# Kernel optimization log

Measured on AMD Instinct MI355X. Metric: run time of the kernel, lower is better.

Reference implementation:

```python
import jax, jax.numpy as jnp
import numpy as np

N, NFEAT, NHID, NCLASS = 10000, 512, 256, 16
CRF_ITERS = 3


def setup_inputs() -> dict:
    key = jax.random.key(0)
    ks = jax.random.split(key, 10)
    x = jax.random.normal(ks[0], (N, NFEAT), dtype=jnp.float32)
    # sparse-ish adjacency: ~50 neighbors/node, self-loops, row-normalized (GCN style)
    mask = (jax.random.uniform(ks[1], (N, N)) < 0.005).astype(jnp.float32)
    adj = mask + jnp.eye(N, dtype=jnp.float32)
    adj = adj / jnp.sum(adj, axis=1, keepdims=True)
    s1 = 1.0 / np.sqrt(NFEAT)
    s2 = 1.0 / np.sqrt(NHID)
    W1 = jax.random.normal(ks[2], (NFEAT, NHID), dtype=jnp.float32) * s1
    b1 = jnp.zeros((NHID,), dtype=jnp.float32)
    Wq = jax.random.normal(ks[3], (NHID, NHID), dtype=jnp.float32) * s2
    Wk = jax.random.normal(ks[4], (NHID, NHID), dtype=jnp.float32) * s2
    alpha = jnp.float32(1.0)
    beta = jnp.float32(1.0)
    ln_w = jnp.ones((NHID,), dtype=jnp.float32)
    ln_b = jnp.zeros((NHID,), dtype=jnp.float32)
    W2 = jax.random.normal(ks[5], (NHID, NCLASS), dtype=jnp.float32) * s2
    b2 = jnp.zeros((NCLASS,), dtype=jnp.float32)
    return {"x": x, "adj": adj, "W1": W1, "b1": b1, "Wq": Wq, "Wk": Wk,
            "alpha": alpha, "beta": beta, "ln_w": ln_w, "ln_b": ln_b,
            "W2": W2, "b2": b2}


def reference(x, adj, W1, b1, Wq, Wk, alpha, beta, ln_w, ln_b, W2, b2):
    # gc1: adj @ (x W1) + b1, then relu
    h = jax.nn.relu(adj @ (x @ W1) + b1)          # [N, NHID]
    # CRF_Node: adjacency-masked similarity attention, 3 mean-field iterations
    q = h @ Wq
    k = h @ Wk
    scores = (q @ k.T) / jnp.sqrt(jnp.float32(NHID))  # [N, N]
    logits = jnp.where(adj > 0, scores, jnp.float32(-1e9))
    attn = jax.nn.softmax(logits, axis=-1)
    out = h
    for _ in range(CRF_ITERS):
        out = (alpha * h + beta * (attn @ out)) / (alpha + beta)
    # LayerNorm over feature dim
    mu = jnp.mean(out, axis=-1, keepdims=True)
    var = jnp.var(out, axis=-1, keepdims=True)
    out = (out - mu) * jax.lax.rsqrt(var + 1e-5) * ln_w + ln_b
    # dropout: eval mode (identity)
    # gc2 + log_softmax
    y = adj @ (out @ W2) + b2                     # [N, NCLASS]
    return jax.nn.log_softmax(y, axis=-1)
```

## Files before the change

kernel.cpp:

```cpp
#include <hip/hip_runtime.h>
#include <math.h>
#include <float.h>

#define N_NODES 10000
#define NFEAT   512
#define NHID    256
#define NCLASS  16
#define CAP     128

typedef float nfloat4 __attribute__((ext_vector_type(4)));

__global__ __launch_bounds__(256) void gemm64(const float* __restrict__ A,
                                              const float* __restrict__ B,
                                              float* __restrict__ C,
                                              int M, int K, int N) {
  __shared__ float As[16][68];
  __shared__ float Bs[16][68];
  const int tid  = threadIdx.x;
  const int row0 = blockIdx.x * 64;
  const int col0 = blockIdx.y * 64;
  const int ty = tid >> 4, tx = tid & 15;
  const int arow = tid >> 2;
  const int akq  = (tid & 3) << 2;
  const int brow = tid >> 4;
  const int bcol = (tid & 15) << 2;

  float acc[4][4] = {};
  for (int k0 = 0; k0 < K; k0 += 16) {
    float4 av = make_float4(0.f, 0.f, 0.f, 0.f);
    const int gr = row0 + arow;
    if (gr < M) av = *(const float4*)&A[(size_t)gr * K + k0 + akq];
    As[akq + 0][arow] = av.x;
    As[akq + 1][arow] = av.y;
    As[akq + 2][arow] = av.z;
    As[akq + 3][arow] = av.w;
    const float4 bv = *(const float4*)&B[(size_t)(k0 + brow) * N + col0 + bcol];
    *(float4*)&Bs[brow][bcol] = bv;
    __syncthreads();
#pragma unroll
    for (int k = 0; k < 16; ++k) {
      const float4 a = *(const float4*)&As[k][ty << 2];
      const float4 b = *(const float4*)&Bs[k][tx << 2];
      acc[0][0] += a.x * b.x; acc[0][1] += a.x * b.y; acc[0][2] += a.x * b.z; acc[0][3] += a.x * b.w;
      acc[1][0] += a.y * b.x; acc[1][1] += a.y * b.y; acc[1][2] += a.y * b.z; acc[1][3] += a.y * b.w;
      acc[2][0] += a.z * b.x; acc[2][1] += a.z * b.y; acc[2][2] += a.z * b.z; acc[2][3] += a.z * b.w;
      acc[3][0] += a.w * b.x; acc[3][1] += a.w * b.y; acc[3][2] += a.w * b.z; acc[3][3] += a.w * b.w;
    }
    __syncthreads();
  }
#pragma unroll
  for (int j = 0; j < 4; ++j) {
    const int gr = row0 + (ty << 2) + j;
    if (gr < M) {
      const float4 o = make_float4(acc[j][0], acc[j][1], acc[j][2], acc[j][3]);
      *(float4*)&C[(size_t)gr * N + col0 + (tx << 2)] = o;
    }
  }
}

__global__ __launch_bounds__(256) void wqwkT(const float* __restrict__ Wq,
                                             const float* __restrict__ Wk,
                                             float* __restrict__ Mm) {
  __shared__ float4 qr4[NHID / 4];
  const int a = blockIdx.x, tid = threadIdx.x;
  if (tid < NHID / 4) qr4[tid] = ((const float4*)&Wq[(size_t)a * NHID])[tid];
  __syncthreads();
  const float4* kb = (const float4*)&Wk[(size_t)tid * NHID];
  float acc = 0.f;
#pragma unroll 8
  for (int c4 = 0; c4 < NHID / 4; ++c4) {
    const float4 k4 = kb[c4];
    const float4 q4 = qr4[c4];
    acc += q4.x * k4.x + q4.y * k4.y + q4.z * k4.z + q4.w * k4.w;
  }
  Mm[(size_t)a * NHID + tid] = acc;
}

__global__ __launch_bounds__(256) void scan_build(const float* __restrict__ adj,
                                                  const float* __restrict__ xW1,
                                                  const float* __restrict__ b1,
                                                  int* __restrict__ cols,
                                                  float* __restrict__ vals,
                                                  int* __restrict__ nnz,
                                                  float* __restrict__ h) {
  __shared__ int    lcols[CAP];
  __shared__ float  lvals[CAP];
  __shared__ int    scols[CAP];
  __shared__ float  svals[CAP];
  __shared__ float4 pacc[4][64];
  __shared__ int    cnt;
  const int row = blockIdx.x, tid = threadIdx.x;
  if (tid == 0) cnt = 0;
  __syncthreads();
  const nfloat4* arow = (const nfloat4*)&adj[(size_t)row * N_NODES];
  for (int v = tid; v < N_NODES / 4; v += 256) {
    const nfloat4 f = __builtin_nontemporal_load(&arow[v]);
    if (f.x != 0.f) { int p = atomicAdd(&cnt, 1); if (p < CAP) { lcols[p] = 4 * v + 0; lvals[p] = f.x; } }
    if (f.y != 0.f) { int p = atomicAdd(&cnt, 1); if (p < CAP) { lcols[p] = 4 * v + 1; lvals[p] = f.y; } }
    if (f.z != 0.f) { int p = atomicAdd(&cnt, 1); if (p < CAP) { lcols[p] = 4 * v + 2; lvals[p] = f.z; } }
    if (f.w != 0.f) { int p = atomicAdd(&cnt, 1); if (p < CAP) { lcols[p] = 4 * v + 3; lvals[p] = f.w; } }
  }
  __syncthreads();
  const int c = min(cnt, CAP);
  int myc = 0; float myv = 0.f; int rank = 0;
  if (tid < c) {
    myc = lcols[tid]; myv = lvals[tid];
    for (int e = 0; e < c; ++e) rank += (lcols[e] < myc);
  }
  __syncthreads();
  if (tid < c) { scols[rank] = myc; svals[rank] = myv; }
  __syncthreads();
  if (tid == 0) nnz[row] = c;
  if (tid < c) {
    cols[(size_t)row * CAP + tid] = scols[tid];
    vals[(size_t)row * CAP + tid] = svals[tid];
  }
  const int lane = tid & 63, wv = tid >> 6;
  float4 acc = make_float4(0.f, 0.f, 0.f, 0.f);
  for (int e = wv; e < c; e += 4) {
    const float vv = svals[e];
    const float4 xv = *(const float4*)&xW1[(size_t)scols[e] * NHID + (lane << 2)];
    acc.x += vv * xv.x; acc.y += vv * xv.y; acc.z += vv * xv.z; acc.w += vv * xv.w;
  }
  pacc[wv][lane] = acc;
  __syncthreads();
  if (wv == 0) {
    const float4 p0 = pacc[0][lane], p1 = pacc[1][lane];
    const float4 p2 = pacc[2][lane], p3 = pacc[3][lane];
    const float4 bb = *(const float4*)&b1[lane << 2];
    float4 r;
    r.x = fmaxf(bb.x + ((p0.x + p1.x) + (p2.x + p3.x)), 0.f);
    r.y = fmaxf(bb.y + ((p0.y + p1.y) + (p2.y + p3.y)), 0.f);
    r.z = fmaxf(bb.z + ((p0.z + p1.z) + (p2.z + p3.z)), 0.f);
    r.w = fmaxf(bb.w + ((p0.w + p1.w) + (p2.w + p3.w)), 0.f);
    *(float4*)&h[(size_t)row * NHID + (lane << 2)] = r;
  }
}

__global__ __launch_bounds__(256) void attn_crf1(const float* __restrict__ t,
                                                 const float* __restrict__ h,
                                                 const int* __restrict__ cols,
                                                 const int* __restrict__ nnz,
                                                 float* __restrict__ attn,
                                                 float* __restrict__ outn,
                                                 const float* __restrict__ alpha_p,
                                                 const float* __restrict__ beta_p) {
  __shared__ int   lcols[4][CAP];
  __shared__ float sv[4][CAP];
  const int tid = threadIdx.x, lane = tid & 63, wv = tid >> 6;
  const int row = (blockIdx.x << 2) + wv;
  const int c = nnz[row];
  for (int e = lane; e < c; e += 64) lcols[wv][e] = cols[(size_t)row * CAP + e];
  const int gq = lane >> 4, gl = lane & 15;
  const float* tp = &t[(size_t)row * NHID + (gl << 2)];
  const float4 t0 = *(const float4*)&tp[0];
  const float4 t1 = *(const float4*)&tp[64];
  const float4 t2 = *(const float4*)&tp[128];
  const float4 t3 = *(const float4*)&tp[192];
  for (int e = gq; e < c; e += 4) {
    const float* hp = &h[(size_t)lcols[wv][e] * NHID + (gl << 2)];
    const float4 h0 = *(const float4*)&hp[0];
    const float4 h1 = *(const float4*)&hp[64];
    const float4 h2 = *(const float4*)&hp[128];
    const float4 h3 = *(const float4*)&hp[192];
    float p = t0.x * h0.x + t0.y * h0.y + t0.z * h0.z + t0.w * h0.w
            + t1.x * h1.x + t1.y * h1.y + t1.z * h1.z + t1.w * h1.w
            + t2.x * h2.x + t2.y * h2.y + t2.z * h2.z + t2.w * h2.w
            + t3.x * h3.x + t3.y * h3.y + t3.z * h3.z + t3.w * h3.w;
    p += __shfl_xor(p, 1, 64);
    p += __shfl_xor(p, 2, 64);
    p += __shfl_xor(p, 4, 64);
    p += __shfl_xor(p, 8, 64);
    if (gl == 0) sv[wv][e] = p * 0.0625f;
  }
  const float s1 = (lane      < c) ? sv[wv][lane]      : -FLT_MAX;
  const float s2 = (lane + 64 < c) ? sv[wv][lane + 64] : -FLT_MAX;
  float m = fmaxf(s1, s2);
#pragma unroll
  for (int o = 32; o > 0; o >>= 1) m = fmaxf(m, __shfl_xor(m, o, 64));
  const float e1 = (lane      < c) ? __expf(s1 - m) : 0.f;
  const float e2 = (lane + 64 < c) ? __expf(s2 - m) : 0.f;
  float sum = e1 + e2;
#pragma unroll
  for (int o = 32; o > 0; o >>= 1) sum += __shfl_xor(sum, o, 64);
  const float inv = 1.f / sum;
  if (lane < c) {
    const float aw = e1 * inv;
    sv[wv][lane] = aw;
    attn[(size_t)row * CAP + lane] = aw;
  }
  if (lane + 64 < c) {
    const float aw = e2 * inv;
    sv[wv][lane + 64] = aw;
    attn[(size_t)row * CAP + lane + 64] = aw;
  }
  float4 acc = make_float4(0.f, 0.f, 0.f, 0.f);
  for (int e = 0; e < c; ++e) {
    const float ve = sv[wv][e];
    const float4 xv = *(const float4*)&h[(size_t)lcols[wv][e] * NHID + (lane << 2)];
    acc.x += ve * xv.x; acc.y += ve * xv.y; acc.z += ve * xv.z; acc.w += ve * xv.w;
  }
  const float a = alpha_p[0], b = beta_p[0];
  const float i2 = 1.f / (a + b);
  const float4 hq = *(const float4*)&h[(size_t)row * NHID + (lane << 2)];
  float4 o4;
  o4.x = (a * hq.x + b * acc.x) * i2;
  o4.y = (a * hq.y + b * acc.y) * i2;
  o4.z = (a * hq.z + b * acc.z) * i2;
  o4.w = (a * hq.w + b * acc.w) * i2;
  *(float4*)&outn[(size_t)row * NHID + (lane << 2)] = o4;
}

__global__ __launch_bounds__(256) void crf_iter(const float* __restrict__ h,
                                                const float* __restrict__ attn,
                                                const int* __restrict__ cols,
                                                const int* __restrict__ nnz,
                                                const float* __restrict__ outp,
                                                float* __restrict__ outn,
                                                const float* __restrict__ alpha_p,
                                                const float* __restrict__ beta_p) {
  __shared__ int   lcols[4][CAP];
  __shared__ float lv[4][CAP];
  const int tid = threadIdx.x, lane = tid & 63, wv = tid >> 6;
  const int row = (blockIdx.x << 2) + wv;
  const int c = nnz[row];
  for (int e = lane; e < c; e += 64) {
    lcols[wv][e] = cols[(size_t)row * CAP + e];
    lv[wv][e]   = attn[(size_t)row * CAP + e];
  }
  float4 acc = make_float4(0.f, 0.f, 0.f, 0.f);
  int e = 0;
  for (; e + 1 < c; e += 2) {
    const int   c0 = lcols[wv][e],   c1 = lcols[wv][e + 1];
    const float v0 = lv[wv][e],      v1 = lv[wv][e + 1];
    const float4 x0 = *(const float4*)&outp[(size_t)c0 * NHID + (lane << 2)];
    const float4 x1 = *(const float4*)&outp[(size_t)c1 * NHID + (lane << 2)];
    acc.x += v0 * x0.x; acc.y += v0 * x0.y; acc.z += v0 * x0.z; acc.w += v0 * x0.w;
    acc.x += v1 * x1.x; acc.y += v1 * x1.y; acc.z += v1 * x1.z; acc.w += v1 * x1.w;
  }
  if (e < c) {
    const float ve = lv[wv][e];
    const float4 xv = *(const float4*)&outp[(size_t)lcols[wv][e] * NHID + (lane << 2)];
    acc.x += ve * xv.x; acc.y += ve * xv.y; acc.z += ve * xv.z; acc.w += ve * xv.w;
  }
  const float a = alpha_p[0], b = beta_p[0];
  const float i2 = 1.f / (a + b);
  const float4 hq = *(const float4*)&h[(size_t)row * NHID + (lane << 2)];
  float4 o4;
  o4.x = (a * hq.x + b * acc.x) * i2;
  o4.y = (a * hq.y + b * acc.y) * i2;
  o4.z = (a * hq.z + b * acc.z) * i2;
  o4.w = (a * hq.w + b * acc.w) * i2;
  *(float4*)&outn[(size_t)row * NHID + (lane << 2)] = o4;
}

__global__ __launch_bounds__(256) void crf_ln_w2(const float* __restrict__ h,
                                                 const float* __restrict__ attn,
                                                 const int* __restrict__ cols,
                                                 const int* __restrict__ nnz,
                                                 const float* __restrict__ outp,
                                                 const float* __restrict__ alpha_p,
                                                 const float* __restrict__ beta_p,
                                                 const float* __restrict__ lnw,
                                                 const float* __restrict__ lnb,
                                                 const float* __restrict__ W2,
                                                 float* __restrict__ z) {
  __shared__ int   lcols[4][CAP];
  __shared__ float lv[4][CAP];
  __shared__ float vs[4][NHID];
  __shared__ float part[16][17];
  const int tid = threadIdx.x, lane = tid & 63, wv = tid >> 6;
  const int row = (blockIdx.x << 2) + wv;
  const int c = nnz[row];
  for (int e = lane; e < c; e += 64) {
    lcols[wv][e] = cols[(size_t)row * CAP + e];
    lv[wv][e]   = attn[(size_t)row * CAP + e];
  }
  float4 acc = make_float4(0.f, 0.f, 0.f, 0.f);
  for (int e = 0; e < c; ++e) {
    const float ve = lv[wv][e];
    const float4 xv = *(const float4*)&outp[(size_t)lcols[wv][e] * NHID + (lane << 2)];
    acc.x += ve * xv.x; acc.y += ve * xv.y; acc.z += ve * xv.z; acc.w += ve * xv.w;
  }
  const float a = alpha_p[0], b = beta_p[0];
  const float i2 = 1.f / (a + b);
  const float4 hq = *(const float4*)&h[(size_t)row * NHID + (lane << 2)];
  float4 x4;
  x4.x = (a * hq.x + b * acc.x) * i2;
  x4.y = (a * hq.y + b * acc.y) * i2;
  x4.z = (a * hq.z + b * acc.z) * i2;
  x4.w = (a * hq.w + b * acc.w) * i2;
  float s = x4.x + x4.y + x4.z + x4.w;
#pragma unroll
  for (int o = 32; o > 0; o >>= 1) s += __shfl_xor(s, o, 64);
  const float mu = s * (1.f / NHID);
  float4 d4;
  d4.x = x4.x - mu; d4.y = x4.y - mu; d4.z = x4.z - mu; d4.w = x4.w - mu;
  float v = d4.x * d4.x + d4.y * d4.y + d4.z * d4.z + d4.w * d4.w;
#pragma unroll
  for (int o = 32; o > 0; o >>= 1) v += __shfl_xor(v, o, 64);
  const float rstd = rsqrtf(v * (1.f / NHID) + 1e-5f);
  const float4 lw = *(const float4*)&lnw[lane << 2];
  const float4 lb = *(const float4*)&lnb[lane << 2];
  float4 v4;
  v4.x = d4.x * rstd * lw.x + lb.x;
  v4.y = d4.y * rstd * lw.y + lb.y;
  v4.z = d4.z * rstd * lw.z + lb.z;
  v4.w = d4.w * rstd * lw.w + lb.w;
  *(float4*)&vs[wv][lane << 2] = v4;
  __syncthreads();
  const int g = tid >> 4, cc = tid & 15;
  float w2f[16];
#pragma unroll
  for (int u = 0; u < 16; ++u) w2f[u] = W2[(size_t)((g << 4) + u) * NCLASS + cc];
  for (int rr = 0; rr < 4; ++rr) {
    float p = 0.f;
#pragma unroll
    for (int u = 0; u < 16; ++u) p += vs[rr][(g << 4) + u] * w2f[u];
    part[g][cc] = p;
    __syncthreads();
    if (tid < NCLASS) {
      float q = 0.f;
#pragma unroll
      for (int g2 = 0; g2 < 16; ++g2) q += part[g2][tid];
      z[(size_t)((blockIdx.x << 2) + rr) * NCLASS + tid] = q;
    }
    __syncthreads();
  }
}

__global__ __launch_bounds__(256) void final_k(const float* __restrict__ z,
                                               const float* __restrict__ vals,
                                               const int* __restrict__ cols,
                                               const int* __restrict__ nnz,
                                               const float* __restrict__ b2,
                                               float* __restrict__ out) {
  __shared__ int   lcols[4][CAP];
  __shared__ float lv[4][CAP];
  const int tid = threadIdx.x, lane = tid & 63, wv = tid >> 6;
  const int row = (blockIdx.x << 2) + wv;
  const int c = nnz[row];
  for (int e = lane; e < c; e += 64) {
    lcols[wv][e] = cols[(size_t)row * CAP + e];
    lv[wv][e]   = vals[(size_t)row * CAP + e];
  }
  const int eg = lane >> 4, cc = lane & 15;
  float acc = 0.f;
  for (int e = eg; e < c; e += 4)
    acc += lv[wv][e] * z[(size_t)lcols[wv][e] * NCLASS + cc];
  acc += __shfl_xor(acc, 16, 64);
  acc += __shfl_xor(acc, 32, 64);
  const float y = acc + b2[cc];
  float m = y;
#pragma unroll
  for (int o = 8; o > 0; o >>= 1) m = fmaxf(m, __shfl_xor(m, o, 64));
  const float ev = __expf(y - m);
  float sme = ev;
#pragma unroll
  for (int o = 8; o > 0; o >>= 1) sme += __shfl_xor(sme, o, 64);
  if (eg == 0) out[(size_t)row * NCLASS + cc] = y - m - logf(sme);
}

extern "C" void kernel_launch(void* const* d_in, const int* in_sizes, int n_in,
                              void* d_out, int out_size, void* d_ws, size_t ws_size,
                              hipStream_t stream) {
  const float* x   = (const float*)d_in[0];
  const float* adj = (const float*)d_in[1];
  const float* W1  = (const float*)d_in[2];
  const float* b1  = (const float*)d_in[3];
  const float* Wq  = (const float*)d_in[4];
  const float* Wk  = (const float*)d_in[5];
  const float* al  = (const float*)d_in[6];
  const float* be  = (const float*)d_in[7];
  const float* lnw = (const float*)d_in[8];
  const float* lnb = (const float*)d_in[9];
  const float* W2  = (const float*)d_in[10];
  const float* b2  = (const float*)d_in[11];
  float* out = (float*)d_out;

  char* w = (char*)d_ws;
  size_t off = 0;
  auto alloc = [&](size_t bytes) -> void* {
    void* p = (void*)(w + off);
    off += (bytes + 255) & ~(size_t)255;
    return p;
  };
  float* bufA = (float*)alloc(sizeof(float) * N_NODES * NHID);
  float* h    = (float*)alloc(sizeof(float) * N_NODES * NHID);
  float* outA = (float*)alloc(sizeof(float) * N_NODES * NHID);
  float* Mm   = (float*)alloc(sizeof(float) * NHID * NHID);
  float* z    = (float*)alloc(sizeof(float) * N_NODES * NCLASS);
  int*   cols = (int*)  alloc(sizeof(int)   * N_NODES * CAP);
  float* vals = (float*)alloc(sizeof(float) * N_NODES * CAP);
  float* attn = (float*)alloc(sizeof(float) * N_NODES * CAP);
  int*   nnz  = (int*)  alloc(sizeof(int)   * N_NODES);
  float* xW1  = bufA;
  float* t    = bufA;
  float* outB = bufA;

  const dim3 gg((N_NODES + 63) / 64, NHID / 64);
  const int rb = N_NODES / 4;

  gemm64<<<gg, 256, 0, stream>>>(x, W1, xW1, N_NODES, NFEAT, NHID);
  wqwkT<<<NHID, 256, 0, stream>>>(Wq, Wk, Mm);
  scan_build<<<N_NODES, 256, 0, stream>>>(adj, xW1, b1, cols, vals, nnz, h);
  gemm64<<<gg, 256, 0, stream>>>(h, Mm, t, N_NODES, NHID, NHID);
  attn_crf1<<<rb, 256, 0, stream>>>(t, h, cols, nnz, attn, outA, al, be);
  crf_iter<<<rb, 256, 0, stream>>>(h, attn, cols, nnz, outA, outB, al, be);
  crf_ln_w2<<<rb, 256, 0, stream>>>(h, attn, cols, nnz, outB, al, be,
                                    lnw, lnb, W2, z);
  final_k<<<rb, 256, 0, stream>>>(z, vals, cols, nnz, b2, out);
}
```

Baseline: 840.2 us.

## Fuse score, softmax and first aggregation into one online-softmax pass

Replaces the two-pass attention kernel (score gather with 16-lane groups, then softmax, then a second gather of neighbor rows for aggregation) with a single loop that loads each neighbor row once, computes the dot product via a full 64-lane shuffle reduction, and updates a running max/sum/accumulator flash-style. This halves the gathered neighbor-row reads. In exchange each edge now takes a serial 6-step shuffle reduction plus two exps per lane, and the loop runs one edge at a time instead of four in parallel.

Result: no change. 831.9 us (-1.0%).

```diff
diff --git a/kernel.cpp b/kernel.cpp
--- a/kernel.cpp
+++ b/kernel.cpp
@@ -151,63 +151,37 @@
   const int row = (blockIdx.x << 2) + wv;
   const int c = nnz[row];
   for (int e = lane; e < c; e += 64) lcols[wv][e] = cols[(size_t)row * CAP + e];
-  const int gq = lane >> 4, gl = lane & 15;
-  const float* tp = &t[(size_t)row * NHID + (gl << 2)];
-  const float4 t0 = *(const float4*)&tp[0];
-  const float4 t1 = *(const float4*)&tp[64];
-  const float4 t2 = *(const float4*)&tp[128];
-  const float4 t3 = *(const float4*)&tp[192];
-  for (int e = gq; e < c; e += 4) {
-    const float* hp = &h[(size_t)lcols[wv][e] * NHID + (gl << 2)];
-    const float4 h0 = *(const float4*)&hp[0];
-    const float4 h1 = *(const float4*)&hp[64];
-    const float4 h2 = *(const float4*)&hp[128];
-    const float4 h3 = *(const float4*)&hp[192];
-    float p = t0.x * h0.x + t0.y * h0.y + t0.z * h0.z + t0.w * h0.w
-            + t1.x * h1.x + t1.y * h1.y + t1.z * h1.z + t1.w * h1.w
-            + t2.x * h2.x + t2.y * h2.y + t2.z * h2.z + t2.w * h2.w
-            + t3.x * h3.x + t3.y * h3.y + t3.z * h3.z + t3.w * h3.w;
-    p += __shfl_xor(p, 1, 64);
-    p += __shfl_xor(p, 2, 64);
-    p += __shfl_xor(p, 4, 64);
-    p += __shfl_xor(p, 8, 64);
-    if (gl == 0) sv[wv][e] = p * 0.0625f;
-  }
-  const float s1 = (lane      < c) ? sv[wv][lane]      : -FLT_MAX;
-  const float s2 = (lane + 64 < c) ? sv[wv][lane + 64] : -FLT_MAX;
-  float m = fmaxf(s1, s2);
-#pragma unroll
-  for (int o = 32; o > 0; o >>= 1) m = fmaxf(m, __shfl_xor(m, o, 64));
-  const float e1 = (lane      < c) ? __expf(s1 - m) : 0.f;
-  const float e2 = (lane + 64 < c) ? __expf(s2 - m) : 0.f;
-  float sum = e1 + e2;
-#pragma unroll
-  for (int o = 32; o > 0; o >>= 1) sum += __shfl_xor(sum, o, 64);
-  const float inv = 1.f / sum;
-  if (lane < c) {
-    const float aw = e1 * inv;
-    sv[wv][lane] = aw;
-    attn[(size_t)row * CAP + lane] = aw;
-  }
-  if (lane + 64 < c) {
-    const float aw = e2 * inv;
-    sv[wv][lane + 64] = aw;
-    attn[(size_t)row * CAP + lane + 64] = aw;
-  }
+  const float4 tq = *(const float4*)&t[(size_t)row * NHID + (lane << 2)];
+  float m = -FLT_MAX, l = 0.f;
   float4 acc = make_float4(0.f, 0.f, 0.f, 0.f);
   for (int e = 0; e < c; ++e) {
-    const float ve = sv[wv][e];
-    const float4 xv = *(const float4*)&h[(size_t)lcols[wv][e] * NHID + (lane << 2)];
-    acc.x += ve * xv.x; acc.y += ve * xv.y; acc.z += ve * xv.z; acc.w += ve * xv.w;
-  }
+    const float4 h4 = *(const float4*)&h[(size_t)lcols[wv][e] * NHID + (lane << 2)];
+    float p = tq.x * h4.x + tq.y * h4.y + tq.z * h4.z + tq.w * h4.w;
+#pragma unroll
+    for (int o = 1; o < 64; o <<= 1) p += __shfl_xor(p, o, 64);
+    const float s = p * 0.0625f;
+    if (lane == 0) sv[wv][e] = s;
+    const float m_new = fmaxf(m, s);
+    const float scale = __expf(m - m_new);
+    const float w     = __expf(s - m_new);
+    l = l * scale + w;
+    acc.x = acc.x * scale + w * h4.x;
+    acc.y = acc.y * scale + w * h4.y;
+    acc.z = acc.z * scale + w * h4.z;
+    acc.w = acc.w * scale + w * h4.w;
+    m = m_new;
+  }
+  const float invl = 1.f / l;
+  if (lane < c)      attn[(size_t)row * CAP + lane]      = __expf(sv[wv][lane]      - m) * invl;
+  if (lane + 64 < c) attn[(size_t)row * CAP + lane + 64] = __expf(sv[wv][lane + 64] - m) * invl;
   const float a = alpha_p[0], b = beta_p[0];
   const float i2 = 1.f / (a + b);
   const float4 hq = *(const float4*)&h[(size_t)row * NHID + (lane << 2)];
   float4 o4;
-  o4.x = (a * hq.x + b * acc.x) * i2;
-  o4.y = (a * hq.y + b * acc.y) * i2;
-  o4.z = (a * hq.z + b * acc.z) * i2;
-  o4.w = (a * hq.w + b * acc.w) * i2;
+  o4.x = (a * hq.x + b * acc.x * invl) * i2;
+  o4.y = (a * hq.y + b * acc.y * invl) * i2;
+  o4.z = (a * hq.z + b * acc.z * invl) * i2;
+  o4.w = (a * hq.w + b * acc.w * invl) * i2;
   *(float4*)&outn[(size_t)row * NHID + (lane << 2)] = o4;
 }
 
```
